# Performance work log

Measured on AMD Instinct MI355X. Metric: run time of the kernel, lower is better.

## Reference

```python
import jax, jax.numpy as jnp
import numpy as np

ND, NA, E, EL, H, F = 100000, 50000, 500000, 200000, 128, 128


def setup_inputs() -> dict:
    key = jax.random.key(0)
    ks = jax.random.split(key, 20)
    def W(k, shape):
        return jax.random.normal(k, shape, dtype=jnp.float32) * 0.05
    inp = {
        'doc_x': jax.random.normal(ks[0], (ND, F), dtype=jnp.float32),
        'author_node_id': jnp.arange(NA, dtype=jnp.int64 if jax.config.jax_enable_x64 else jnp.int32),
        'edge_index': jnp.stack([
            jax.random.randint(ks[1], (E,), 0, ND),   # doc src
            jax.random.randint(ks[2], (E,), 0, NA),   # author dst
        ]),
        'edge_label_index': jnp.stack([
            jax.random.randint(ks[3], (EL,), 0, ND),
            jax.random.randint(ks[4], (EL,), 0, NA),
        ]),
        'doc_lin_W': W(ks[5], (F, H)), 'doc_lin_b': W(ks[6], (H,)),
        'author_emb': W(ks[7], (NA, H)),
        'c1_da_Wl': W(ks[8], (H, H)), 'c1_da_bl': W(ks[9], (H,)), 'c1_da_Wr': W(ks[10], (H, H)),
        'c1_ad_Wl': W(ks[11], (H, H)), 'c1_ad_bl': W(ks[12], (H,)), 'c1_ad_Wr': W(ks[13], (H, H)),
        'c2_da_Wl': W(ks[14], (H, H)), 'c2_da_bl': W(ks[15], (H,)), 'c2_da_Wr': W(ks[16], (H, H)),
        'c2_ad_Wl': W(ks[17], (H, H)), 'c2_ad_bl': W(ks[18], (H,)), 'c2_ad_Wr': W(ks[19], (H, H)),
    }
    return inp


def sage(x_src, x_dst, src, dst, num_dst, Wl, bl, Wr):
    # PyG SAGEConv (aggr='mean'): lin_l(mean_j x_src[j]) + lin_r(x_dst)
    msg = x_src[src]                                            # [E, H]
    agg = jax.ops.segment_sum(msg, dst, num_segments=num_dst)   # [num_dst, H]
    deg = jax.ops.segment_sum(jnp.ones_like(dst, dtype=x_src.dtype), dst, num_segments=num_dst)
    agg = agg / jnp.maximum(deg, 1.0)[:, None]
    return agg @ Wl + bl + x_dst @ Wr


def reference(doc_x, author_node_id, edge_index, edge_label_index,
              doc_lin_W, doc_lin_b, author_emb,
              c1_da_Wl, c1_da_bl, c1_da_Wr, c1_ad_Wl, c1_ad_bl, c1_ad_Wr,
              c2_da_Wl, c2_da_bl, c2_da_Wr, c2_ad_Wl, c2_ad_bl, c2_ad_Wr):
    x_doc = doc_x @ doc_lin_W + doc_lin_b          # [ND, H]
    x_author = author_emb[author_node_id]          # [NA, H]
    src_d, dst_a = edge_index[0], edge_index[1]
    # layer 1 (per-edge-type convs, to_hetero semantics) + ReLU
    h_a = sage(x_doc, x_author, src_d, dst_a, NA, c1_da_Wl, c1_da_bl, c1_da_Wr)
    h_d = sage(x_author, x_doc, dst_a, src_d, ND, c1_ad_Wl, c1_ad_bl, c1_ad_Wr)
    h_a, h_d = jax.nn.relu(h_a), jax.nn.relu(h_d)
    # layer 2
    o_a = sage(h_d, h_a, src_d, dst_a, NA, c2_da_Wl, c2_da_bl, c2_da_Wr)
    o_d = sage(h_a, h_d, dst_a, src_d, ND, c2_ad_Wl, c2_ad_bl, c2_ad_Wr)
    # edge scorer: dot product of gathered endpoint embeddings
    pred = (o_d[edge_label_index[0]] * o_a[edge_label_index[1]]).sum(-1)  # [EL]
    return pred
```

## Files before the change

kernel.cpp:

```cpp
#include <hip/hip_runtime.h>

typedef unsigned short u16;
typedef __attribute__((ext_vector_type(8))) short vbf16x8;
typedef __attribute__((ext_vector_type(4))) float vf32x4;

__device__ __forceinline__ float bf2f(u16 u) {
    union { unsigned int i; float f; } v; v.i = ((unsigned int)u) << 16; return v.f;
}
__device__ __forceinline__ u16 f2bf(float f) {
    union { float f; unsigned int i; } v; v.f = f;
    return (u16)((v.i + 0x7fffu + ((v.i >> 16) & 1u)) >> 16);
}

struct TPack { const float* src[9]; u16* dst[9]; };

#define NBUK 256
#define NBLK_BIN 256
#define SCAP 24
#define OVFCAP 32768
#define PACK_SH 17

__global__ __launch_bounds__(256) void wtp(TPack p, int* __restrict__ ovfn) {
    int b = blockIdx.x;
    if (b == 0 && threadIdx.x < 2) ovfn[threadIdx.x] = 0;
    int mat = b >> 6;
    const float* s = p.src[mat];
    u16* d = p.dst[mat];
    int i = (b & 63) * 256 + threadIdx.x;
    int k = i >> 7, n = i & 127;
    d[(size_t)n * 128 + k] = f2bf(s[(size_t)k * 128 + n]);
}

__global__ __launch_bounds__(256) void mega2(
    const float* __restrict__ A1f, const u16* __restrict__ W1T,
    const float* __restrict__ biasd, u16* __restrict__ xdoc, int M, int BD,
    const float* __restrict__ emb, const int* __restrict__ ids,
    u16* __restrict__ xauth, int NA,
    const int* __restrict__ src, const int* __restrict__ dst,
    unsigned* __restrict__ stageD, unsigned* __restrict__ stageA,
    int* __restrict__ cntD, int* __restrict__ cntA,
    uint2* __restrict__ ovfD, uint2* __restrict__ ovfA, int* __restrict__ ovfn,
    int E, int shD, int shA) {
    __shared__ u16 WS[128 * 128];
    const int b = blockIdx.x;
    const int tid = threadIdx.x;

    if (b < BD) {
        const int lane = tid & 63, wave = tid >> 6;
        const int r15 = lane & 15, kq = lane >> 4;
        const int rowbase = b * 128 + wave * 32;
        const int m0 = rowbase + r15, m1 = rowbase + 16 + r15;
        const bool v0 = rowbase < M, v1 = rowbase + 16 < M;

        vf32x4 acc0[8], acc1[8];
#pragma unroll
        for (int i = 0; i < 8; ++i) { acc0[i] = (vf32x4)(0.0f); acc1[i] = (vf32x4)(0.0f); }

#pragma unroll
        for (int i = 0; i < 8; ++i) {
            int L = i * 256 + tid;
            int n = L >> 4, bk = L & 15;
            *(uint4*)(WS + ((size_t)n * 16 + (bk ^ (n & 15))) * 8) =
                *(const uint4*)(W1T + (size_t)L * 8);
        }
        __syncthreads();

#pragma unroll
        for (int ks = 0; ks < 4; ++ks) {
            vbf16x8 a0 = (vbf16x8)(short)0, a1 = (vbf16x8)(short)0;
            if (v0) {
                const float* p = A1f + (size_t)m0 * 128 + ks * 32 + kq * 8;
                float4 lo = *(const float4*)p, hi = *(const float4*)(p + 4);
                a0[0] = (short)f2bf(lo.x); a0[1] = (short)f2bf(lo.y);
                a0[2] = (short)f2bf(lo.z); a0[3] = (short)f2bf(lo.w);
                a0[4] = (short)f2bf(hi.x); a0[5] = (short)f2bf(hi.y);
                a0[6] = (short)f2bf(hi.z); a0[7] = (short)f2bf(hi.w);
            }
            if (v1) {
                const float* p = A1f + (size_t)m1 * 128 + ks * 32 + kq * 8;
                float4 lo = *(const float4*)p, hi = *(const float4*)(p + 4);
                a1[0] = (short)f2bf(lo.x); a1[1] = (short)f2bf(lo.y);
                a1[2] = (short)f2bf(lo.z); a1[3] = (short)f2bf(lo.w);
                a1[4] = (short)f2bf(hi.x); a1[5] = (short)f2bf(hi.y);
                a1[6] = (short)f2bf(hi.z); a1[7] = (short)f2bf(hi.w);
            }
#pragma unroll
            for (int nt = 0; nt < 8; ++nt) {
                vbf16x8 bb = *(const vbf16x8*)(
                    WS + ((size_t)(nt * 16 + r15) * 16 + ((ks * 4 + kq) ^ r15)) * 8);
                acc0[nt] = __builtin_amdgcn_mfma_f32_16x16x32_bf16(a0, bb, acc0[nt], 0, 0, 0);
                acc1[nt] = __builtin_amdgcn_mfma_f32_16x16x32_bf16(a1, bb, acc1[nt], 0, 0, 0);
            }
        }

#pragma unroll
        for (int nt = 0; nt < 8; ++nt) {
            const float bv = biasd[nt * 16 + r15];
#pragma unroll
            for (int r = 0; r < 4; ++r) {
                if (v0) xdoc[(size_t)(rowbase + kq * 4 + r) * 128 + nt * 16 + r15] =
                    f2bf(acc0[nt][r] + bv);
                if (v1) xdoc[(size_t)(rowbase + 16 + kq * 4 + r) * 128 + nt * 16 + r15] =
                    f2bf(acc1[nt][r] + bv);
            }
        }
        return;
    }

    if (b < BD + 2 * NBLK_BIN) {
        int* lcnt = (int*)WS;
        int bb = b - BD;
        const bool isD = bb < NBLK_BIN;
        const int blk = isD ? bb : bb - NBLK_BIN;
        const int* key = isD ? src : dst;
        const int* val = isD ? dst : src;
        const int shift = isD ? shD : shA;
        unsigned* stage = isD ? stageD : stageA;
        int* cnt = isD ? cntD : cntA;
        uint2* ovf = isD ? ovfD : ovfA;
        int* on = ovfn + (isD ? 0 : 1);
        const int per = (E + NBLK_BIN - 1) / NBLK_BIN;
        const int beg = blk * per;
        const int end = min(beg + per, E);
        for (int i = tid; i < NBUK; i += 256) lcnt[i] = 0;
        __syncthreads();
        for (int e = beg + tid; e < end; e += 256) {
            int k = key[e], v = val[e];
            int bkt = k >> shift;
            int slot = atomicAdd(&lcnt[bkt], 1);
            if (slot < SCAP) {
                unsigned local = (unsigned)(k - (bkt << shift));
                stage[((size_t)bkt * NBLK_BIN + blk) * SCAP + slot] =
                    (local << PACK_SH) | (unsigned)v;
            } else {
                int oi = atomicAdd(on, 1);
                if (oi < OVFCAP) ovf[oi] = make_uint2((unsigned)k, (unsigned)v);
            }
        }
        __syncthreads();
        for (int i = tid; i < NBUK; i += 256)
            cnt[(size_t)i * NBLK_BIN + blk] = min(lcnt[i], SCAP);
        return;
    }

    int gid = (b - BD - 2 * NBLK_BIN) * 256 + tid;
    if (gid >= NA * 16) return;
    int n = gid >> 4, f = gid & 15;
    int id = ids[n];
    const float* s = emb + (size_t)id * 128 + f * 8;
    float4 lo = *(const float4*)(s);
    float4 hi = *(const float4*)(s + 4);
    u16 o[8] = {f2bf(lo.x), f2bf(lo.y), f2bf(lo.z), f2bf(lo.w),
                f2bf(hi.x), f2bf(hi.y), f2bf(hi.z), f2bf(hi.w)};
    *(uint4*)(xauth + (size_t)n * 128 + f * 8) = *(const uint4*)o;
}

__global__ __launch_bounds__(256) void bucket_count2(
    const unsigned* __restrict__ stageD, const unsigned* __restrict__ stageA,
    const int* __restrict__ cntD, const int* __restrict__ cntA,
    const uint2* __restrict__ ovfD, const uint2* __restrict__ ovfA,
    const int* __restrict__ ovfn,
    int* __restrict__ cnt_d, int* __restrict__ cnt_a, int* __restrict__ btot,
    int ND, int NA, int shD, int shA) {
    __shared__ int hist[1024];
    __shared__ int segc[NBLK_BIN];
    __shared__ int red[256];
    const bool isD = (int)blockIdx.x < NBUK;
    const int b = isD ? (int)blockIdx.x : (int)blockIdx.x - NBUK;
    const int sh = isD ? shD : shA;
    const int N = isD ? ND : NA;
    const int base = b << sh;
    const int range = min(1 << sh, N - base);
    const int tid = threadIdx.x;
    if (range <= 0) { if (tid == 0) btot[blockIdx.x] = 0; return; }
    const unsigned* stage = (isD ? stageD : stageA) + (size_t)b * NBLK_BIN * SCAP;
    const int* scnt = (isD ? cntD : cntA) + (size_t)b * NBLK_BIN;
    const uint2* ovf = isD ? ovfD : ovfA;
    const int nov = min(ovfn[isD ? 0 : 1], OVFCAP);
    int* out = isD ? cnt_d : cnt_a;
    for (int i = tid; i < (1 << sh); i += 256) hist[i] = 0;
    segc[tid] = scnt[tid];
    __syncthreads();
    int my = 0;
    for (int j = tid; j < NBLK_BIN * SCAP; j += 256) {
        int seg = j / SCAP, slot = j - seg * SCAP;
        if (slot < segc[seg]) { atomicAdd(&hist[stage[j] >> PACK_SH], 1); ++my; }
    }
    for (int i = tid; i < nov; i += 256) {
        int k = (int)ovf[i].x;
        if ((k >> sh) == b) { atomicAdd(&hist[k - base], 1); ++my; }
    }
    red[tid] = my;
    __syncthreads();
    for (int s = 128; s > 0; s >>= 1) {
        if (tid < s) red[tid] += red[tid + s];
        __syncthreads();
    }
    if (tid == 0) btot[blockIdx.x] = red[0];
    for (int i = tid; i < range; i += 256) out[base + i] = hist[i];
}

__global__ __launch_bounds__(256) void scanb(int* __restrict__ btot) {
    __shared__ int sh[256];
    const int tid = threadIdx.x;
    for (int seg = 0; seg < 2; ++seg) {
        int* p = btot + seg * NBUK;
        int v = p[tid];
        sh[tid] = v;
        __syncthreads();
        for (int off = 1; off < 256; off <<= 1) {
            int t = tid >= off ? sh[tid - off] : 0;
            __syncthreads();
            sh[tid] += t;
            __syncthreads();
        }
        p[tid] = sh[tid] - v;
        __syncthreads();
    }
}

__global__ __launch_bounds__(256) void bucket_fill3(
    const unsigned* __restrict__ stageD, const unsigned* __restrict__ stageA,
    const int* __restrict__ cntD, const int* __restrict__ cntA,
    const uint2* __restrict__ ovfD, const uint2* __restrict__ ovfA,
    const int* __restrict__ ovfn,
    const int* __restrict__ cnt_d, const int* __restrict__ cnt_a,
    const int* __restrict__ btot,
    int* __restrict__ offs_d, int* __restrict__ offs_a,
    int* __restrict__ nbr_d, int* __restrict__ nbr_a,
    int ND, int NA, int shD, int shA) {
    __shared__ int lcur[1024];
    __shared__ int segc[NBLK_BIN];
    __shared__ int sh[256];
    __shared__ int carry;
    const bool isD = (int)blockIdx.x < NBUK;
    const int b = isD ? (int)blockIdx.x : (int)blockIdx.x - NBUK;
    const int shft = isD ? shD : shA;
    const int N = isD ? ND : NA;
    const int base = b << shft;
    const int range = min(1 << shft, N - base);
    if (range <= 0) return;
    const unsigned* stage = (isD ? stageD : stageA) + (size_t)b * NBLK_BIN * SCAP;
    const int* scnt = (isD ? cntD : cntA) + (size_t)b * NBLK_BIN;
    const uint2* ovf = isD ? ovfD : ovfA;
    const int nov = min(ovfn[isD ? 0 : 1], OVFCAP);
    const int* cnodes = isD ? cnt_d : cnt_a;
    int* offs = isD ? offs_d : offs_a;
    int* nbr = isD ? nbr_d : nbr_a;
    const int tid = threadIdx.x;
    segc[tid] = scnt[tid];
    if (tid == 0) carry = btot[blockIdx.x];
    __syncthreads();
    for (int c0 = 0; c0 < range; c0 += 256) {
        int i = c0 + tid;
        int v = (i < range) ? cnodes[base + i] : 0;
        sh[tid] = v;
        __syncthreads();
        for (int off = 1; off < 256; off <<= 1) {
            int t = tid >= off ? sh[tid - off] : 0;
            __syncthreads();
            sh[tid] += t;
            __syncthreads();
        }
        if (i < range) {
            int ex = carry + sh[tid] - v;
            lcur[i] = ex;
            offs[base + i] = ex;
        }
        __syncthreads();
        if (tid == 255) carry += sh[255];
        __syncthreads();
    }
    if (tid == 0) offs[base + range] = carry;
    __syncthreads();
    for (int j = tid; j < NBLK_BIN * SCAP; j += 256) {
        int seg = j / SCAP, slot = j - seg * SCAP;
        if (slot < segc[seg]) {
            unsigned pk = stage[j];
            int local = pk >> PACK_SH;
            int v = (int)(pk & ((1u << PACK_SH) - 1u));
            nbr[atomicAdd(&lcur[local], 1)] = v;
        }
    }
    for (int i = tid; i < nov; i += 256) {
        int k = (int)ovf[i].x;
        if ((k >> shft) == b)
            nbr[atomicAdd(&lcur[k - base], 1)] = (int)ovf[i].y;
    }
}

__global__ __launch_bounds__(256) void agg_mean2(
    const u16* __restrict__ xa, const int* __restrict__ offs_a,
    const int* __restrict__ nbr_a, u16* __restrict__ outa, int NA,
    const u16* __restrict__ xd, const int* __restrict__ offs_d,
    const int* __restrict__ nbr_d, u16* __restrict__ outd, int ND) {
    int gid = blockIdx.x * 256 + threadIdx.x;
    int node = gid >> 4, f = gid & 15;
    int lane = threadIdx.x & 63;
    int gbase = lane & 48;
    const u16* x; const int* offs; const int* nbr; u16* out;
    if (node < NA) { x = xa; offs = offs_a; nbr = nbr_a; out = outa; }
    else {
        node -= NA;
        if (node >= ND) return;
        x = xd; offs = offs_d; nbr = nbr_d; out = outd;
    }
    int beg = offs[node], end = offs[node + 1];
    float acc[8] = {0, 0, 0, 0, 0, 0, 0, 0};

    for (int i = beg; i < end; i += 16) {
        int cnt = end - i; if (cnt > 16) cnt = 16;
        int myn = (i + f < end) ? nbr[i + f] : 0;
        int t = 0;
        for (; t + 3 < cnt; t += 4) {
            int i0 = __shfl(myn, gbase + t);
            int i1 = __shfl(myn, gbase + t + 1);
            int i2 = __shfl(myn, gbase + t + 2);
            int i3 = __shfl(myn, gbase + t + 3);
            uint4 q0 = *(const uint4*)(x + (size_t)i0 * 128 + f * 8);
            uint4 q1 = *(const uint4*)(x + (size_t)i1 * 128 + f * 8);
            uint4 q2 = *(const uint4*)(x + (size_t)i2 * 128 + f * 8);
            uint4 q3 = *(const uint4*)(x + (size_t)i3 * 128 + f * 8);
            acc[0] += bf2f((u16)(q0.x & 0xffff)) + bf2f((u16)(q1.x & 0xffff))
                    + bf2f((u16)(q2.x & 0xffff)) + bf2f((u16)(q3.x & 0xffff));
            acc[1] += bf2f((u16)(q0.x >> 16))    + bf2f((u16)(q1.x >> 16))
                    + bf2f((u16)(q2.x >> 16))    + bf2f((u16)(q3.x >> 16));
            acc[2] += bf2f((u16)(q0.y & 0xffff)) + bf2f((u16)(q1.y & 0xffff))
                    + bf2f((u16)(q2.y & 0xffff)) + bf2f((u16)(q3.y & 0xffff));
            acc[3] += bf2f((u16)(q0.y >> 16))    + bf2f((u16)(q1.y >> 16))
                    + bf2f((u16)(q2.y >> 16))    + bf2f((u16)(q3.y >> 16));
            acc[4] += bf2f((u16)(q0.z & 0xffff)) + bf2f((u16)(q1.z & 0xffff))
                    + bf2f((u16)(q2.z & 0xffff)) + bf2f((u16)(q3.z & 0xffff));
            acc[5] += bf2f((u16)(q0.z >> 16))    + bf2f((u16)(q1.z >> 16))
                    + bf2f((u16)(q2.z >> 16))    + bf2f((u16)(q3.z >> 16));
            acc[6] += bf2f((u16)(q0.w & 0xffff)) + bf2f((u16)(q1.w & 0xffff))
                    + bf2f((u16)(q2.w & 0xffff)) + bf2f((u16)(q3.w & 0xffff));
            acc[7] += bf2f((u16)(q0.w >> 16))    + bf2f((u16)(q1.w >> 16))
                    + bf2f((u16)(q2.w >> 16))    + bf2f((u16)(q3.w >> 16));
        }
        for (; t < cnt; ++t) {
            int i0 = __shfl(myn, gbase + t);
            uint4 q0 = *(const uint4*)(x + (size_t)i0 * 128 + f * 8);
            acc[0] += bf2f((u16)(q0.x & 0xffff));
            acc[1] += bf2f((u16)(q0.x >> 16));
            acc[2] += bf2f((u16)(q0.y & 0xffff));
            acc[3] += bf2f((u16)(q0.y >> 16));
            acc[4] += bf2f((u16)(q0.z & 0xffff));
            acc[5] += bf2f((u16)(q0.z >> 16));
            acc[6] += bf2f((u16)(q0.w & 0xffff));
            acc[7] += bf2f((u16)(q0.w >> 16));
        }
    }
    float inv = 1.0f / fmaxf((float)(end - beg), 1.0f);
    u16 o[8];
#pragma unroll
    for (int j = 0; j < 8; ++j) o[j] = f2bf(acc[j] * inv);
    *(uint4*)(out + (size_t)node * 128 + f * 8) = *(const uint4*)o;
}

struct SideParams3 {
    const u16* A1b; const u16* W1T;
    const u16* A2b; const u16* W2T;
    const float* bias; u16* out;
    int M; int do_relu; int ntiles; int gblocks;
};
__global__ __launch_bounds__(256) void conv_gemm3(SideParams3 sa, SideParams3 sd) {
    __shared__ u16 WS[2 * 128 * 128];
    const bool isA = (int)blockIdx.x < sa.gblocks;
    SideParams3 P = isA ? sa : sd;
    const int gb = isA ? (int)blockIdx.x : (int)blockIdx.x - sa.gblocks;
    const int tid = threadIdx.x;
    const int lane = tid & 63, wave = tid >> 6;
    const int r15 = lane & 15, kq = lane >> 4;

#pragma unroll
    for (int i = 0; i < 8; ++i) {
        int L = i * 256 + tid;
        int n = L >> 4, bk = L & 15;
        *(uint4*)(WS + ((size_t)n * 16 + (bk ^ (n & 15))) * 8) =
            *(const uint4*)(P.W1T + (size_t)L * 8);
        *(uint4*)(WS + 16384 + ((size_t)n * 16 + (bk ^ (n & 15))) * 8) =
            *(const uint4*)(P.W2T + (size_t)L * 8);
    }
    __syncthreads();
    float bv[8];
#pragma unroll
    for (int nt = 0; nt < 8; ++nt) bv[nt] = P.bias[nt * 16 + r15];

    auto loadA = [&](const u16* Ab, int tile, vbf16x8* fa, vbf16x8* fb) {
        const int rowbase = tile * 128 + wave * 32;
        const int m0 = rowbase + r15, m1 = rowbase + 16 + r15;
        const bool v0 = rowbase < P.M, v1 = rowbase + 16 < P.M;
#pragma unroll
        for (int ks = 0; ks < 4; ++ks) {
            fa[ks] = v0 ? *(const vbf16x8*)(Ab + (size_t)m0 * 128 + ks * 32 + kq * 8)
                        : (vbf16x8)(short)0;
            fb[ks] = v1 ? *(const vbf16x8*)(Ab + (size_t)m1 * 128 + ks * 32 + kq * 8)
                        : (vbf16x8)(short)0;
        }
    };

    vbf16x8 c1a[4], c1b[4], c2a[4], c2b[4], n1a[4], n1b[4];
    if (gb < P.ntiles) loadA(P.A1b, gb, c1a, c1b);
    for (int t = gb; t < P.ntiles; t += P.gblocks) {
        loadA(P.A2b, t, c2a, c2b);
        const int tn = t + P.gblocks;
        if (tn < P.ntiles) loadA(P.A1b, tn, n1a, n1b);

        vf32x4 acc0[8], acc1[8];
#pragma unroll
        for (int i = 0; i < 8; ++i) { acc0[i] = (vf32x4)(0.0f); acc1[i] = (vf32x4)(0.0f); }
#pragma unroll
        for (int ks = 0; ks < 4; ++ks) {
#pragma unroll
            for (int nt = 0; nt < 8; ++nt) {
                vbf16x8 b = *(const vbf16x8*)(
                    WS + ((size_t)(nt * 16 + r15) * 16 + ((ks * 4 + kq) ^ r15)) * 8);
                acc0[nt] = __builtin_amdgcn_mfma_f32_16x16x32_bf16(c1a[ks], b, acc0[nt], 0, 0, 0);
                acc1[nt] = __builtin_amdgcn_mfma_f32_16x16x32_bf16(c1b[ks], b, acc1[nt], 0, 0, 0);
            }
        }
#pragma unroll
        for (int ks = 0; ks < 4; ++ks) {
#pragma unroll
            for (int nt = 0; nt < 8; ++nt) {
                vbf16x8 b = *(const vbf16x8*)(
                    WS + 16384 + ((size_t)(nt * 16 + r15) * 16 + ((ks * 4 + kq) ^ r15)) * 8);
                acc0[nt] = __builtin_amdgcn_mfma_f32_16x16x32_bf16(c2a[ks], b, acc0[nt], 0, 0, 0);
                acc1[nt] = __builtin_amdgcn_mfma_f32_16x16x32_bf16(c2b[ks], b, acc1[nt], 0, 0, 0);
            }
        }

        const int rowbase = t * 128 + wave * 32;
        const bool v0 = rowbase < P.M, v1 = rowbase + 16 < P.M;
#pragma unroll
        for (int nt = 0; nt < 8; ++nt) {
#pragma unroll
            for (int r = 0; r < 4; ++r) {
                if (v0) {
                    float v = acc0[nt][r] + bv[nt];
                    if (P.do_relu) v = fmaxf(v, 0.0f);
                    P.out[(size_t)(rowbase + kq * 4 + r) * 128 + nt * 16 + r15] = f2bf(v);
                }
                if (v1) {
                    float v = acc1[nt][r] + bv[nt];
                    if (P.do_relu) v = fmaxf(v, 0.0f);
                    P.out[(size_t)(rowbase + 16 + kq * 4 + r) * 128 + nt * 16 + r15] = f2bf(v);
                }
            }
        }
#pragma unroll
        for (int ks = 0; ks < 4; ++ks) { c1a[ks] = n1a[ks]; c1b[ks] = n1b[ks]; }
    }
}

__global__ __launch_bounds__(256) void edge_dot(
    const u16* __restrict__ od, const u16* __restrict__ oa,
    const int* __restrict__ i0, const int* __restrict__ i1,
    float* __restrict__ pred, int EL) {
    int gid = blockIdx.x * 256 + threadIdx.x;
    if (gid >= EL * 16) return;
    int e = gid >> 4, f = gid & 15;
    uint4 x = *(const uint4*)(od + (size_t)i0[e] * 128 + f * 8);
    uint4 y = *(const uint4*)(oa + (size_t)i1[e] * 128 + f * 8);
    float s = 0.0f;
    s += bf2f((u16)(x.x & 0xffff)) * bf2f((u16)(y.x & 0xffff));
    s += bf2f((u16)(x.x >> 16))    * bf2f((u16)(y.x >> 16));
    s += bf2f((u16)(x.y & 0xffff)) * bf2f((u16)(y.y & 0xffff));
    s += bf2f((u16)(x.y >> 16))    * bf2f((u16)(y.y >> 16));
    s += bf2f((u16)(x.z & 0xffff)) * bf2f((u16)(y.z & 0xffff));
    s += bf2f((u16)(x.z >> 16))    * bf2f((u16)(y.z >> 16));
    s += bf2f((u16)(x.w & 0xffff)) * bf2f((u16)(y.w & 0xffff));
    s += bf2f((u16)(x.w >> 16))    * bf2f((u16)(y.w >> 16));
    s += __shfl_xor(s, 1);
    s += __shfl_xor(s, 2);
    s += __shfl_xor(s, 4);
    s += __shfl_xor(s, 8);
    if (f == 0) pred[e] = s;
}

extern "C" void kernel_launch(void* const* d_in, const int* in_sizes, int n_in,
                              void* d_out, int out_size, void* d_ws, size_t ws_size,
                              hipStream_t stream) {
    const float* doc_x    = (const float*)d_in[0];
    const int*   auth_id  = (const int*)d_in[1];
    const int*   eidx     = (const int*)d_in[2];
    const int*   elidx    = (const int*)d_in[3];
    const float* W_doc    = (const float*)d_in[4];
    const float* b_doc    = (const float*)d_in[5];
    const float* emb      = (const float*)d_in[6];
    const float* c1_da_Wl = (const float*)d_in[7];
    const float* c1_da_bl = (const float*)d_in[8];
    const float* c1_da_Wr = (const float*)d_in[9];
    const float* c1_ad_Wl = (const float*)d_in[10];
    const float* c1_ad_bl = (const float*)d_in[11];
    const float* c1_ad_Wr = (const float*)d_in[12];
    const float* c2_da_Wl = (const float*)d_in[13];
    const float* c2_da_bl = (const float*)d_in[14];
    const float* c2_da_Wr = (const float*)d_in[15];
    const float* c2_ad_Wl = (const float*)d_in[16];
    const float* c2_ad_bl = (const float*)d_in[17];
    const float* c2_ad_Wr = (const float*)d_in[18];

    const int ND = in_sizes[0] / 128;
    const int NA = in_sizes[1];
    const int E  = in_sizes[2] / 2;
    const int EL = in_sizes[3] / 2;
    const int* e_src = eidx;
    const int* e_dst = eidx + E;
    const int BA = (NA + 127) / 128, BD = (ND + 127) / 128;
    const int gatherB = (NA * 16 + 255) / 256;

    char* base = (char*)d_ws;
    size_t off = 0;
    auto alloc = [&](size_t bytes) {
        void* p = base + off;
        off = (off + bytes + 255) & ~(size_t)255;
        return p;
    };
    u16*  xdoc  = (u16*)alloc((size_t)ND * 128 * 2);
    u16*  xauth = (u16*)alloc((size_t)NA * 128 * 2);
    u16*  hd    = (u16*)alloc((size_t)ND * 128 * 2);
    u16*  ha    = (u16*)alloc((size_t)NA * 128 * 2);
    u16*  aggA  = (u16*)alloc((size_t)NA * 128 * 2);
    u16*  aggD  = (u16*)alloc((size_t)ND * 128 * 2);
    u16*  wt    = (u16*)alloc((size_t)9 * 128 * 128 * 2);
    int*  cnt   = (int*)alloc((size_t)(ND + NA) * 4);
    int*  offs_d = (int*)alloc((size_t)(ND + 1) * 4);
    int*  offs_a = (int*)alloc((size_t)(NA + 1) * 4);
    int*  nbr_d = (int*)alloc((size_t)E * 4);
    int*  nbr_a = (int*)alloc((size_t)E * 4);
    int*  cntD  = (int*)alloc((size_t)NBUK * NBLK_BIN * 4);
    int*  cntA  = (int*)alloc((size_t)NBUK * NBLK_BIN * 4);
    int*  btot  = (int*)alloc((size_t)2 * NBUK * 4);
    uint2* ovfD = (uint2*)alloc((size_t)OVFCAP * 8);
    uint2* ovfA = (uint2*)alloc((size_t)OVFCAP * 8);
    int*  ovfn  = (int*)alloc(256);
    (void)ws_size; (void)n_in; (void)out_size;
    u16* od = xdoc;
    u16* oa = xauth;
    unsigned* stageD = (unsigned*)aggD;
    unsigned* stageA = (unsigned*)aggA;

    TPack tp;
    const float* srcs[9] = {W_doc, c1_da_Wl, c1_da_Wr, c1_ad_Wl, c1_ad_Wr,
                            c2_da_Wl, c2_da_Wr, c2_ad_Wl, c2_ad_Wr};
    for (int i = 0; i < 9; ++i) { tp.src[i] = srcs[i]; tp.dst[i] = wt + (size_t)i * 16384; }
    const u16 *WTdoc = wt, *WT_c1daL = wt + 16384, *WT_c1daR = wt + 2 * 16384,
              *WT_c1adL = wt + 3 * 16384, *WT_c1adR = wt + 4 * 16384,
              *WT_c2daL = wt + 5 * 16384, *WT_c2daR = wt + 6 * 16384,
              *WT_c2adL = wt + 7 * 16384, *WT_c2adR = wt + 8 * 16384;

    int shD = 0; while (((ND - 1) >> shD) >= NBUK) ++shD;
    int shA = 0; while (((NA - 1) >> shA) >= NBUK) ++shA;

    wtp<<<576, 256, 0, stream>>>(tp, ovfn);

    mega2<<<BD + 2 * NBLK_BIN + gatherB, 256, 0, stream>>>(
        doc_x, WTdoc, b_doc, xdoc, ND, BD,
        emb, auth_id, xauth, NA,
        e_src, e_dst, stageD, stageA, cntD, cntA, ovfD, ovfA, ovfn,
        E, shD, shA);

    bucket_count2<<<2 * NBUK, 256, 0, stream>>>(
        stageD, stageA, cntD, cntA, ovfD, ovfA, ovfn,
        cnt, cnt + ND, btot, ND, NA, shD, shA);

    scanb<<<1, 256, 0, stream>>>(btot);

    bucket_fill3<<<2 * NBUK, 256, 0, stream>>>(
        stageD, stageA, cntD, cntA, ovfD, ovfA, ovfn,
        cnt, cnt + ND, btot, offs_d, offs_a, nbr_d, nbr_a,
        ND, NA, shD, shA);

    const int aggGrid = ((NA + ND) * 16 + 255) / 256;
    const int gA = (int)(((long)512 * BA) / (BA + BD));
    const int gD = 512 - gA;

    agg_mean2<<<aggGrid, 256, 0, stream>>>(
        xdoc, offs_a, nbr_a, aggA, NA, xauth, offs_d, nbr_d, aggD, ND);
    {
        SideParams3 sa = {aggA, WT_c1daL, xauth, WT_c1daR, c1_da_bl, ha, NA, 1, BA, gA};
        SideParams3 sd = {aggD, WT_c1adL, xdoc,  WT_c1adR, c1_ad_bl, hd, ND, 1, BD, gD};
        conv_gemm3<<<gA + gD, 256, 0, stream>>>(sa, sd);
    }

    agg_mean2<<<aggGrid, 256, 0, stream>>>(
        hd, offs_a, nbr_a, aggA, NA, ha, offs_d, nbr_d, aggD, ND);
    {
        SideParams3 sa = {aggA, WT_c2daL, ha, WT_c2daR, c2_da_bl, oa, NA, 0, BA, gA};
        SideParams3 sd = {aggD, WT_c2adL, hd, WT_c2adR, c2_ad_bl, od, ND, 0, BD, gD};
        conv_gemm3<<<gA + gD, 256, 0, stream>>>(sa, sd);
    }

    edge_dot<<<(EL * 16 + 255) / 256, 256, 0, stream>>>(
        od, oa, elidx, elidx + EL, (float*)d_out, EL);
}
```

Measured before the change: 354.8 us.

## Interleave GEMM, binning and gather blocks in mega2; fold bucket scan into fill

The mega2 kernel now maps block indices proportionally across its three roles (doc GEMM tiles, edge-binning blocks, author gather), so the different workloads are interleaved across the grid instead of running in contiguous ranges. The separate single-block scanb launch is removed. Each bucket_fill3 block instead computes its own exclusive prefix by summing the preceding bucket totals with a shared-memory reduction. This saves one kernel launch and its serialization, and aims to balance compute-bound and memory-bound blocks across CUs, at the cost of redundant per-block summation and 64-bit index arithmetic.

```diff
diff --git a/kernel.cpp b/kernel.cpp
--- a/kernel.cpp
+++ b/kernel.cpp
@@ -35,20 +35,25 @@
     const float* __restrict__ A1f, const u16* __restrict__ W1T,
     const float* __restrict__ biasd, u16* __restrict__ xdoc, int M, int BD,
     const float* __restrict__ emb, const int* __restrict__ ids,
-    u16* __restrict__ xauth, int NA,
+    u16* __restrict__ xauth, int NA, int gatherB,
     const int* __restrict__ src, const int* __restrict__ dst,
     unsigned* __restrict__ stageD, unsigned* __restrict__ stageA,
     int* __restrict__ cntD, int* __restrict__ cntA,
     uint2* __restrict__ ovfD, uint2* __restrict__ ovfA, int* __restrict__ ovfn,
     int E, int shD, int shA) {
     __shared__ u16 WS[128 * 128];
-    const int b = blockIdx.x;
     const int tid = threadIdx.x;
 
-    if (b < BD) {
+    const long b = blockIdx.x;
+    const long nB = 2 * NBLK_BIN;
+    const long T = (long)BD + nB + gatherB;
+    const long gq0 = (b * BD) / T, gq1 = ((b + 1) * BD) / T;
+
+    if (gq1 > gq0) {
+        const int tile = (int)gq0;
         const int lane = tid & 63, wave = tid >> 6;
         const int r15 = lane & 15, kq = lane >> 4;
-        const int rowbase = b * 128 + wave * 32;
+        const int rowbase = tile * 128 + wave * 32;
         const int m0 = rowbase + r15, m1 = rowbase + 16 + r15;
         const bool v0 = rowbase < M, v1 = rowbase + 16 < M;
 
@@ -107,9 +112,13 @@
         return;
     }
 
-    if (b < BD + 2 * NBLK_BIN) {
+    const long b2 = b - gq0;
+    const long T2 = T - BD;
+    const long bq0 = (b2 * nB) / T2, bq1 = ((b2 + 1) * nB) / T2;
+
+    if (bq1 > bq0) {
         int* lcnt = (int*)WS;
-        int bb = b - BD;
+        int bb = (int)bq0;
         const bool isD = bb < NBLK_BIN;
         const int blk = isD ? bb : bb - NBLK_BIN;
         const int* key = isD ? src : dst;
@@ -143,7 +152,7 @@
         return;
     }
 
-    int gid = (b - BD - 2 * NBLK_BIN) * 256 + tid;
+    int gid = (int)(b2 - bq0) * 256 + tid;
     if (gid >= NA * 16) return;
     int n = gid >> 4, f = gid & 15;
     int id = ids[n];
@@ -200,25 +209,6 @@
     for (int i = tid; i < range; i += 256) out[base + i] = hist[i];
 }
 
-__global__ __launch_bounds__(256) void scanb(int* __restrict__ btot) {
-    __shared__ int sh[256];
-    const int tid = threadIdx.x;
-    for (int seg = 0; seg < 2; ++seg) {
-        int* p = btot + seg * NBUK;
-        int v = p[tid];
-        sh[tid] = v;
-        __syncthreads();
-        for (int off = 1; off < 256; off <<= 1) {
-            int t = tid >= off ? sh[tid - off] : 0;
-            __syncthreads();
-            sh[tid] += t;
-            __syncthreads();
-        }
-        p[tid] = sh[tid] - v;
-        __syncthreads();
-    }
-}
-
 __global__ __launch_bounds__(256) void bucket_fill3(
     const unsigned* __restrict__ stageD, const unsigned* __restrict__ stageA,
     const int* __restrict__ cntD, const int* __restrict__ cntA,
@@ -249,8 +239,19 @@
     int* nbr = isD ? nbr_d : nbr_a;
     const int tid = threadIdx.x;
     segc[tid] = scnt[tid];
-    if (tid == 0) carry = btot[blockIdx.x];
-    __syncthreads();
+    {
+        const int lo = isD ? 0 : NBUK;
+        int acc = 0;
+        for (int j = lo + tid; j < (int)blockIdx.x; j += 256) acc += btot[j];
+        sh[tid] = acc;
+        __syncthreads();
+        for (int s = 128; s > 0; s >>= 1) {
+            if (tid < s) sh[tid] += sh[tid + s];
+            __syncthreads();
+        }
+        if (tid == 0) carry = sh[0];
+        __syncthreads();
+    }
     for (int c0 = 0; c0 < range; c0 += 256) {
         int i = c0 + tid;
         int v = (i < range) ? cnodes[base + i] : 0;
@@ -558,15 +559,13 @@
 
     mega2<<<BD + 2 * NBLK_BIN + gatherB, 256, 0, stream>>>(
         doc_x, WTdoc, b_doc, xdoc, ND, BD,
-        emb, auth_id, xauth, NA,
+        emb, auth_id, xauth, NA, gatherB,
         e_src, e_dst, stageD, stageA, cntD, cntA, ovfD, ovfA, ovfn,
         E, shD, shA);
 
     bucket_count2<<<2 * NBUK, 256, 0, stream>>>(
         stageD, stageA, cntD, cntA, ovfD, ovfA, ovfn,
         cnt, cnt + ND, btot, ND, NA, shD, shA);
-
-    scanb<<<1, 256, 0, stream>>>(btot);
 
     bucket_fill3<<<2 * NBUK, 256, 0, stream>>>(
         stageD, stageA, cntD, cntA, ovfD, ovfA, ovfn,
```

Measured after the change: 360.0 us. No clear change (+1.5%).

## Drop LDS weight staging; read MFMA B fragments directly from global/L2

Applied to the files above, without the earlier changes.

The doc projection GEMM and the conv GEMMs no longer copy the 128x128 bf16 weights into swizzled shared memory. Each wave now loads its B fragments straight from global memory, relying on L2/L1 caching, which removes the LDS fill, the barrier and the large LDS footprint that limited occupancy. The persistent, software-pipelined conv_gemm3 is replaced by a one-tile-per-block conv_nl launched over all tiles, trading the A-prefetch overlap for more blocks in flight. Repeated global weight reads per block may add cache traffic.

```diff
diff --git a/kernel.cpp b/kernel.cpp
--- a/kernel.cpp
+++ b/kernel.cpp
@@ -10,6 +10,10 @@
 __device__ __forceinline__ u16 f2bf(float f) {
     union { float f; unsigned int i; } v; v.f = f;
     return (u16)((v.i + 0x7fffu + ((v.i >> 16) & 1u)) >> 16);
+}
+
+__device__ __forceinline__ vbf16x8 bfrag(const u16* WT, int nt, int r15, int ks, int kq) {
+    return *(const vbf16x8*)(WT + (size_t)(nt * 16 + r15) * 128 + ks * 32 + kq * 8);
 }
 
 struct TPack { const float* src[9]; u16* dst[9]; };
@@ -41,7 +45,7 @@
     int* __restrict__ cntD, int* __restrict__ cntA,
     uint2* __restrict__ ovfD, uint2* __restrict__ ovfA, int* __restrict__ ovfn,
     int E, int shD, int shA) {
-    __shared__ u16 WS[128 * 128];
+    __shared__ int lcnt[NBUK];
     const int b = blockIdx.x;
     const int tid = threadIdx.x;
 
@@ -55,15 +59,6 @@
         vf32x4 acc0[8], acc1[8];
 #pragma unroll
         for (int i = 0; i < 8; ++i) { acc0[i] = (vf32x4)(0.0f); acc1[i] = (vf32x4)(0.0f); }
-
-#pragma unroll
-        for (int i = 0; i < 8; ++i) {
-            int L = i * 256 + tid;
-            int n = L >> 4, bk = L & 15;
-            *(uint4*)(WS + ((size_t)n * 16 + (bk ^ (n & 15))) * 8) =
-                *(const uint4*)(W1T + (size_t)L * 8);
-        }
-        __syncthreads();
 
 #pragma unroll
         for (int ks = 0; ks < 4; ++ks) {
@@ -86,8 +81,7 @@
             }
 #pragma unroll
             for (int nt = 0; nt < 8; ++nt) {
-                vbf16x8 bb = *(const vbf16x8*)(
-                    WS + ((size_t)(nt * 16 + r15) * 16 + ((ks * 4 + kq) ^ r15)) * 8);
+                vbf16x8 bb = bfrag(W1T, nt, r15, ks, kq);
                 acc0[nt] = __builtin_amdgcn_mfma_f32_16x16x32_bf16(a0, bb, acc0[nt], 0, 0, 0);
                 acc1[nt] = __builtin_amdgcn_mfma_f32_16x16x32_bf16(a1, bb, acc1[nt], 0, 0, 0);
             }
@@ -108,7 +102,6 @@
     }
 
     if (b < BD + 2 * NBLK_BIN) {
-        int* lcnt = (int*)WS;
         int bb = b - BD;
         const bool isD = bb < NBLK_BIN;
         const int blk = isD ? bb : bb - NBLK_BIN;
@@ -358,99 +351,61 @@
     *(uint4*)(out + (size_t)node * 128 + f * 8) = *(const uint4*)o;
 }
 
-struct SideParams3 {
+struct SideParams {
     const u16* A1b; const u16* W1T;
     const u16* A2b; const u16* W2T;
     const float* bias; u16* out;
-    int M; int do_relu; int ntiles; int gblocks;
+    int M; int do_relu; int nblocks;
 };
-__global__ __launch_bounds__(256) void conv_gemm3(SideParams3 sa, SideParams3 sd) {
-    __shared__ u16 WS[2 * 128 * 128];
-    const bool isA = (int)blockIdx.x < sa.gblocks;
-    SideParams3 P = isA ? sa : sd;
-    const int gb = isA ? (int)blockIdx.x : (int)blockIdx.x - sa.gblocks;
+__global__ __launch_bounds__(256) void conv_nl(SideParams sa, SideParams sd) {
+    const bool isA = (int)blockIdx.x < sa.nblocks;
+    SideParams P = isA ? sa : sd;
+    const int bx = isA ? blockIdx.x : blockIdx.x - sa.nblocks;
     const int tid = threadIdx.x;
     const int lane = tid & 63, wave = tid >> 6;
     const int r15 = lane & 15, kq = lane >> 4;
-
-#pragma unroll
-    for (int i = 0; i < 8; ++i) {
-        int L = i * 256 + tid;
-        int n = L >> 4, bk = L & 15;
-        *(uint4*)(WS + ((size_t)n * 16 + (bk ^ (n & 15))) * 8) =
-            *(const uint4*)(P.W1T + (size_t)L * 8);
-        *(uint4*)(WS + 16384 + ((size_t)n * 16 + (bk ^ (n & 15))) * 8) =
-            *(const uint4*)(P.W2T + (size_t)L * 8);
-    }
-    __syncthreads();
-    float bv[8];
-#pragma unroll
-    for (int nt = 0; nt < 8; ++nt) bv[nt] = P.bias[nt * 16 + r15];
-
-    auto loadA = [&](const u16* Ab, int tile, vbf16x8* fa, vbf16x8* fb) {
-        const int rowbase = tile * 128 + wave * 32;
-        const int m0 = rowbase + r15, m1 = rowbase + 16 + r15;
-        const bool v0 = rowbase < P.M, v1 = rowbase + 16 < P.M;
+    const int rowbase = bx * 128 + wave * 32;
+    const int m0 = rowbase + r15, m1 = rowbase + 16 + r15;
+    const bool v0 = rowbase < P.M, v1 = rowbase + 16 < P.M;
+
+    vf32x4 acc0[8], acc1[8];
+#pragma unroll
+    for (int i = 0; i < 8; ++i) { acc0[i] = (vf32x4)(0.0f); acc1[i] = (vf32x4)(0.0f); }
+
+#pragma unroll
+    for (int mat = 0; mat < 2; ++mat) {
+        const u16* WT = mat ? P.W2T : P.W1T;
+        const u16* Ab = mat ? P.A2b : P.A1b;
 #pragma unroll
         for (int ks = 0; ks < 4; ++ks) {
-            fa[ks] = v0 ? *(const vbf16x8*)(Ab + (size_t)m0 * 128 + ks * 32 + kq * 8)
-                        : (vbf16x8)(short)0;
-            fb[ks] = v1 ? *(const vbf16x8*)(Ab + (size_t)m1 * 128 + ks * 32 + kq * 8)
-                        : (vbf16x8)(short)0;
-        }
-    };
-
-    vbf16x8 c1a[4], c1b[4], c2a[4], c2b[4], n1a[4], n1b[4];
-    if (gb < P.ntiles) loadA(P.A1b, gb, c1a, c1b);
-    for (int t = gb; t < P.ntiles; t += P.gblocks) {
-        loadA(P.A2b, t, c2a, c2b);
-        const int tn = t + P.gblocks;
-        if (tn < P.ntiles) loadA(P.A1b, tn, n1a, n1b);
-
-        vf32x4 acc0[8], acc1[8];
-#pragma unroll
-        for (int i = 0; i < 8; ++i) { acc0[i] = (vf32x4)(0.0f); acc1[i] = (vf32x4)(0.0f); }
-#pragma unroll
-        for (int ks = 0; ks < 4; ++ks) {
+            vbf16x8 a0 = (vbf16x8)(short)0, a1 = (vbf16x8)(short)0;
+            if (v0) a0 = *(const vbf16x8*)(Ab + (size_t)m0 * 128 + ks * 32 + kq * 8);
+            if (v1) a1 = *(const vbf16x8*)(Ab + (size_t)m1 * 128 + ks * 32 + kq * 8);
 #pragma unroll
             for (int nt = 0; nt < 8; ++nt) {
-                vbf16x8 b = *(const vbf16x8*)(
-                    WS + ((size_t)(nt * 16 + r15) * 16 + ((ks * 4 + kq) ^ r15)) * 8);
-                acc0[nt] = __builtin_amdgcn_mfma_f32_16x16x32_bf16(c1a[ks], b, acc0[nt], 0, 0, 0);
-                acc1[nt] = __builtin_amdgcn_mfma_f32_16x16x32_bf16(c1b[ks], b, acc1[nt], 0, 0, 0);
-            }
-        }
-#pragma unroll
-        for (int ks = 0; ks < 4; ++ks) {
-#pragma unroll
-            for (int nt = 0; nt < 8; ++nt) {
-                vbf16x8 b = *(const vbf16x8*)(
-                    WS + 16384 + ((size_t)(nt * 16 + r15) * 16 + ((ks * 4 + kq) ^ r15)) * 8);
-                acc0[nt] = __builtin_amdgcn_mfma_f32_16x16x32_bf16(c2a[ks], b, acc0[nt], 0, 0, 0);
-                acc1[nt] = __builtin_amdgcn_mfma_f32_16x16x32_bf16(c2b[ks], b, acc1[nt], 0, 0, 0);
-            }
-        }
-
-        const int rowbase = t * 128 + wave * 32;
-        const bool v0 = rowbase < P.M, v1 = rowbase + 16 < P.M;
-#pragma unroll
-        for (int nt = 0; nt < 8; ++nt) {
-#pragma unroll
-            for (int r = 0; r < 4; ++r) {
-                if (v0) {
-                    float v = acc0[nt][r] + bv[nt];
-                    if (P.do_relu) v = fmaxf(v, 0.0f);
-                    P.out[(size_t)(rowbase + kq * 4 + r) * 128 + nt * 16 + r15] = f2bf(v);
-                }
-                if (v1) {
-                    float v = acc1[nt][r] + bv[nt];
-                    if (P.do_relu) v = fmaxf(v, 0.0f);
-                    P.out[(size_t)(rowbase + 16 + kq * 4 + r) * 128 + nt * 16 + r15] = f2bf(v);
-                }
-            }
-        }
-#pragma unroll
-        for (int ks = 0; ks < 4; ++ks) { c1a[ks] = n1a[ks]; c1b[ks] = n1b[ks]; }
+                vbf16x8 b = bfrag(WT, nt, r15, ks, kq);
+                acc0[nt] = __builtin_amdgcn_mfma_f32_16x16x32_bf16(a0, b, acc0[nt], 0, 0, 0);
+                acc1[nt] = __builtin_amdgcn_mfma_f32_16x16x32_bf16(a1, b, acc1[nt], 0, 0, 0);
+            }
+        }
+    }
+
+#pragma unroll
+    for (int nt = 0; nt < 8; ++nt) {
+        const float bv = P.bias[nt * 16 + r15];
+#pragma unroll
+        for (int r = 0; r < 4; ++r) {
+            if (v0) {
+                float v = acc0[nt][r] + bv;
+                if (P.do_relu) v = fmaxf(v, 0.0f);
+                P.out[(size_t)(rowbase + kq * 4 + r) * 128 + nt * 16 + r15] = f2bf(v);
+            }
+            if (v1) {
+                float v = acc1[nt][r] + bv;
+                if (P.do_relu) v = fmaxf(v, 0.0f);
+                P.out[(size_t)(rowbase + 16 + kq * 4 + r) * 128 + nt * 16 + r15] = f2bf(v);
+            }
+        }
     }
 }
 
@@ -574,23 +529,21 @@
         ND, NA, shD, shA);
 
     const int aggGrid = ((NA + ND) * 16 + 255) / 256;
-    const int gA = (int)(((long)512 * BA) / (BA + BD));
-    const int gD = 512 - gA;
 
     agg_mean2<<<aggGrid, 256, 0, stream>>>(
         xdoc, offs_a, nbr_a, aggA, NA, xauth, offs_d, nbr_d, aggD, ND);
     {
-        SideParams3 sa = {aggA, WT_c1daL, xauth, WT_c1daR, c1_da_bl, ha, NA, 1, BA, gA};
-        SideParams3 sd = {aggD, WT_c1adL, xdoc,  WT_c1adR, c1_ad_bl, hd, ND, 1, BD, gD};
-        conv_gemm3<<<gA + gD, 256, 0, stream>>>(sa, sd);
+        SideParams sa = {aggA, WT_c1daL, xauth, WT_c1daR, c1_da_bl, ha, NA, 1, BA};
+        SideParams sd = {aggD, WT_c1adL, xdoc,  WT_c1adR, c1_ad_bl, hd, ND, 1, BD};
+        conv_nl<<<BA + BD, 256, 0, stream>>>(sa, sd);
     }
 
     agg_mean2<<<aggGrid, 256, 0, stream>>>(
         hd, offs_a, nbr_a, aggA, NA, ha, offs_d, nbr_d, aggD, ND);
     {
-        SideParams3 sa = {aggA, WT_c2daL, ha, WT_c2daR, c2_da_bl, oa, NA, 0, BA, gA};
-        SideParams3 sd = {aggD, WT_c2adL, hd, WT_c2adR, c2_ad_bl, od, ND, 0, BD, gD};
-        conv_gemm3<<<gA + gD, 256, 0, stream>>>(sa, sd);
+        SideParams sa = {aggA, WT_c2daL, ha, WT_c2daR, c2_da_bl, oa, NA, 0, BA};
+        SideParams sd = {aggD, WT_c2adL, hd, WT_c2adR, c2_ad_bl, od, ND, 0, BD};
+        conv_nl<<<BA + BD, 256, 0, stream>>>(sa, sd);
     }
 
     edge_dot<<<(EL * 16 + 255) / 256, 256, 0, stream>>>(
```

After: 446.0 us. 25.7% more time.
